# Performance work log

Measured on AMD Instinct MI355X. Metric: run time of the kernel, lower is better.

Reference implementation:

```python
import jax, jax.numpy as jnp
import numpy as np

ALPHA = 0.95   # synaptic current decay, exp(-dt/tau_syn)
BETA = 0.9     # membrane decay, exp(-dt/tau_mem)
THRESHOLD = 0.0


def setup_inputs() -> dict:
    key = jax.random.key(0)
    B, C, H, W, T = 8, 64, 32, 32, 100
    inputs = jax.random.normal(key, (B, C, H, W, T), dtype=jnp.float32)
    return {"inputs": inputs}


def _lif_forward(inputs):
    B, C, H, W, T = inputs.shape
    x = jnp.moveaxis(inputs, -1, 0)  # (T, B, C, H, W): scan over time
    zeros = jnp.zeros((B, C, H, W), dtype=inputs.dtype)

    def step(carry, x_t):
        syn_cur, mem_cur = carry
        # spike when (mem - 1.0) crosses threshold; hard heaviside forward
        out = (mem_cur - 1.0 > THRESHOLD).astype(inputs.dtype)
        syn_next = ALPHA * syn_cur + x_t
        # reset uses detached spike, and accumulates the OLD syn_current
        mem_next = (BETA * mem_cur + syn_cur) * (1.0 - jax.lax.stop_gradient(out))
        return (syn_next, mem_next), (syn_next, mem_next, out)

    _, (syn, mem, spike_out) = jax.lax.scan(step, (zeros, zeros), x)
    # stack back to (B, C, H, W, T)
    syn = jnp.moveaxis(syn, 0, -1)
    mem = jnp.moveaxis(mem, 0, -1)
    spike_out = jnp.moveaxis(spike_out, 0, -1)
    return syn, mem, spike_out


def reference(inputs):
    return _lif_forward(inputs)
```

## Files before the change

kernel.cpp:

```cpp
#include <hip/hip_runtime.h>


typedef float f32x4 __attribute__((ext_vector_type(4)));

constexpr int    T_TOT = 100;
constexpr int    NV4   = 25;
constexpr int    ROW4  = 26;
constexpr int    PPW   = 64;
constexpr double ALPHA = 0.95;
constexpr double BETA  = 0.9;

__device__ __forceinline__ double mul_add_rn64(double a, double b, double c) {
    double p = a * b;
    asm("" : "+v"(p));
    return p + c;
}

#define WAVE_FENCE()  do { __builtin_amdgcn_wave_barrier(); \
                           asm volatile("" ::: "memory"); } while (0)

#define STORE_DENSE(OPTR)                                                     \
    do {                                                                      \
        float* ob = (OPTR) + (size_t)pix0 * T_TOT;                            \
        _Pragma("unroll")                                                     \
        for (int k = 0; k < NV4; ++k) {                                       \
            const int g  = 64 * k + lane;                                     \
            const int ps = g / 25;                                            \
            const int es = g - 25 * ps;                                       \
            const f32x4 v = slab[ps * ROW4 + es];                             \
            *reinterpret_cast<f32x4*>(ob + 4 * (size_t)g) = v;                \
        }                                                                     \
    } while (0)

__global__ __launch_bounds__(64)
void lif_fwd(const float* __restrict__ in,
             float* __restrict__ syn_o,
             float* __restrict__ mem_o,
             float* __restrict__ spk_o)
{
    __shared__ f32x4 slab[PPW * ROW4];

    const int lane = threadIdx.x;
    const int pix0 = blockIdx.x * PPW;
    const float* ib = in + (size_t)pix0 * T_TOT;

    #pragma unroll
    for (int k = 0; k < NV4; ++k) {
        const int g  = 64 * k + lane;
        const f32x4 v = *reinterpret_cast<const f32x4*>(ib + 4 * (size_t)g);
        const int ps = g / 25;
        const int es = g - 25 * ps;
        slab[ps * ROW4 + es] = v;
    }
    WAVE_FENCE();

    double syn = 0.0, mem = 0.0;
    f32x4 mv[NV4];
    unsigned smask[4] = {0u, 0u, 0u, 0u};

    #pragma unroll
    for (int e = 0; e < NV4; ++e) {
        const f32x4 xv = slab[lane * ROW4 + e];
        f32x4 sv;
        {
            #pragma clang fp contract(off)
            #pragma unroll
            for (int j = 0; j < 4; ++j) {
                const int    t     = 4 * e + j;
                const double x     = (double)xv[j];
                const bool   o     = (mem - 1.0 > 0.0);
                const double om    = o ? 0.0 : 1.0;
                const double mem_n = mul_add_rn64(BETA, mem, syn) * om;
                const double syn_n = mul_add_rn64(ALPHA, syn, x);
                sv[j]    = (float)syn_n;
                mv[e][j] = (float)mem_n;
                smask[t >> 5] |= (o ? 1u : 0u) << (t & 31);
                syn = syn_n; mem = mem_n;
            }
        }
        slab[lane * ROW4 + e] = sv;
    }
    WAVE_FENCE();

    STORE_DENSE(syn_o);
    WAVE_FENCE();

    #pragma unroll
    for (int e = 0; e < NV4; ++e) slab[lane * ROW4 + e] = mv[e];
    WAVE_FENCE();
    STORE_DENSE(mem_o);
    WAVE_FENCE();

    #pragma unroll
    for (int e = 0; e < NV4; ++e) {
        f32x4 v;
        #pragma unroll
        for (int j = 0; j < 4; ++j) {
            const int t = 4 * e + j;
            v[j] = ((smask[t >> 5] >> (t & 31)) & 1u) ? 1.0f : 0.0f;
        }
        slab[lane * ROW4 + e] = v;
    }
    WAVE_FENCE();
    STORE_DENSE(spk_o);
}

extern "C" void kernel_launch(void* const* d_in, const int* in_sizes, int n_in,
                              void* d_out, int out_size, void* d_ws, size_t ws_size,
                              hipStream_t stream) {
    const float* in = (const float*)d_in[0];
    float* out = (float*)d_out;

    const int n    = in_sizes[0];
    const int npix = n / T_TOT;

    float* syn_o = out;
    float* mem_o = out + (size_t)n;
    float* spk_o = out + 2 * (size_t)n;

    dim3 grid(npix / PPW);
    dim3 block(64);
    lif_fwd<<<grid, block, 0, stream>>>(in, syn_o, mem_o, spk_o);
}
```

Before: 166.9 us.

## Use persistent grid-stride blocks with register prefetch of next task input

Launches a fixed grid of 2048 single-wave blocks that loop over pixel tasks in grid-stride fashion. Each block loads the next task's input into registers while it runs the recurrence and stores for the current task. The aim is to hide global load latency and reduce block launch overhead. In exchange, register pressure rises from the prefetch buffer and fewer waves are resident, which may reduce latency hiding.

```diff
diff --git a/kernel.cpp b/kernel.cpp
--- a/kernel.cpp
+++ b/kernel.cpp
@@ -36,73 +36,96 @@
 void lif_fwd(const float* __restrict__ in,
              float* __restrict__ syn_o,
              float* __restrict__ mem_o,
-             float* __restrict__ spk_o)
+             float* __restrict__ spk_o,
+             int ntask)
 {
     __shared__ f32x4 slab[PPW * ROW4];
 
-    const int lane = threadIdx.x;
-    const int pix0 = blockIdx.x * PPW;
-    const float* ib = in + (size_t)pix0 * T_TOT;
+    const int lane   = threadIdx.x;
+    const int stride = gridDim.x;
 
-    #pragma unroll
-    for (int k = 0; k < NV4; ++k) {
-        const int g  = 64 * k + lane;
-        const f32x4 v = *reinterpret_cast<const f32x4*>(ib + 4 * (size_t)g);
-        const int ps = g / 25;
-        const int es = g - 25 * ps;
-        slab[ps * ROW4 + es] = v;
+    int task = blockIdx.x;
+    if (task >= ntask) return;
+
+    f32x4 xb[NV4];
+    {
+        const float* ib = in + (size_t)task * PPW * T_TOT;
+        #pragma unroll
+        for (int k = 0; k < NV4; ++k)
+            xb[k] = *reinterpret_cast<const f32x4*>(ib + 4 * (size_t)(64 * k + lane));
     }
-    WAVE_FENCE();
 
-    double syn = 0.0, mem = 0.0;
-    f32x4 mv[NV4];
-    unsigned smask[4] = {0u, 0u, 0u, 0u};
+    for (; task < ntask; task += stride) {
+        const int pix0 = task * PPW;
 
-    #pragma unroll
-    for (int e = 0; e < NV4; ++e) {
-        const f32x4 xv = slab[lane * ROW4 + e];
-        f32x4 sv;
-        {
-            #pragma clang fp contract(off)
+        #pragma unroll
+        for (int k = 0; k < NV4; ++k) {
+            const int g  = 64 * k + lane;
+            const int ps = g / 25;
+            const int es = g - 25 * ps;
+            slab[ps * ROW4 + es] = xb[k];
+        }
+        WAVE_FENCE();
+
+        const int nt = task + stride;
+        if (nt < ntask) {
+            const float* ib = in + (size_t)nt * PPW * T_TOT;
+            #pragma unroll
+            for (int k = 0; k < NV4; ++k)
+                xb[k] = *reinterpret_cast<const f32x4*>(ib + 4 * (size_t)(64 * k + lane));
+        }
+
+        double syn = 0.0, mem = 0.0;
+        f32x4 mv[NV4];
+        unsigned smask[4] = {0u, 0u, 0u, 0u};
+
+        #pragma unroll
+        for (int e = 0; e < NV4; ++e) {
+            const f32x4 xv = slab[lane * ROW4 + e];
+            f32x4 sv;
+            {
+                #pragma clang fp contract(off)
+                #pragma unroll
+                for (int j = 0; j < 4; ++j) {
+                    const int    t     = 4 * e + j;
+                    const double x     = (double)xv[j];
+                    const bool   o     = (mem - 1.0 > 0.0);
+                    const double om    = o ? 0.0 : 1.0;
+                    const double mem_n = mul_add_rn64(BETA, mem, syn) * om;
+                    const double syn_n = mul_add_rn64(ALPHA, syn, x);
+                    sv[j]    = (float)syn_n;
+                    mv[e][j] = (float)mem_n;
+                    smask[t >> 5] |= (o ? 1u : 0u) << (t & 31);
+                    syn = syn_n; mem = mem_n;
+                }
+            }
+            slab[lane * ROW4 + e] = sv;
+        }
+        WAVE_FENCE();
+
+        STORE_DENSE(syn_o);
+        WAVE_FENCE();
+
+        #pragma unroll
+        for (int e = 0; e < NV4; ++e) slab[lane * ROW4 + e] = mv[e];
+        WAVE_FENCE();
+        STORE_DENSE(mem_o);
+        WAVE_FENCE();
+
+        #pragma unroll
+        for (int e = 0; e < NV4; ++e) {
+            f32x4 v;
             #pragma unroll
             for (int j = 0; j < 4; ++j) {
-                const int    t     = 4 * e + j;
-                const double x     = (double)xv[j];
-                const bool   o     = (mem - 1.0 > 0.0);
-                const double om    = o ? 0.0 : 1.0;
-                const double mem_n = mul_add_rn64(BETA, mem, syn) * om;
-                const double syn_n = mul_add_rn64(ALPHA, syn, x);
-                sv[j]    = (float)syn_n;
-                mv[e][j] = (float)mem_n;
-                smask[t >> 5] |= (o ? 1u : 0u) << (t & 31);
-                syn = syn_n; mem = mem_n;
+                const int t = 4 * e + j;
+                v[j] = ((smask[t >> 5] >> (t & 31)) & 1u) ? 1.0f : 0.0f;
             }
+            slab[lane * ROW4 + e] = v;
         }
-        slab[lane * ROW4 + e] = sv;
+        WAVE_FENCE();
+        STORE_DENSE(spk_o);
+        WAVE_FENCE();
     }
-    WAVE_FENCE();
-
-    STORE_DENSE(syn_o);
-    WAVE_FENCE();
-
-    #pragma unroll
-    for (int e = 0; e < NV4; ++e) slab[lane * ROW4 + e] = mv[e];
-    WAVE_FENCE();
-    STORE_DENSE(mem_o);
-    WAVE_FENCE();
-
-    #pragma unroll
-    for (int e = 0; e < NV4; ++e) {
-        f32x4 v;
-        #pragma unroll
-        for (int j = 0; j < 4; ++j) {
-            const int t = 4 * e + j;
-            v[j] = ((smask[t >> 5] >> (t & 31)) & 1u) ? 1.0f : 0.0f;
-        }
-        slab[lane * ROW4 + e] = v;
-    }
-    WAVE_FENCE();
-    STORE_DENSE(spk_o);
 }
 
 extern "C" void kernel_launch(void* const* d_in, const int* in_sizes, int n_in,
@@ -111,14 +134,15 @@
     const float* in = (const float*)d_in[0];
     float* out = (float*)d_out;
 
-    const int n    = in_sizes[0];
-    const int npix = n / T_TOT;
+    const int n     = in_sizes[0];
+    const int npix  = n / T_TOT;
+    const int ntask = npix / PPW;
 
     float* syn_o = out;
     float* mem_o = out + (size_t)n;
     float* spk_o = out + 2 * (size_t)n;
 
-    dim3 grid(npix / PPW);
+    dim3 grid(2048);
     dim3 block(64);
-    lif_fwd<<<grid, block, 0, stream>>>(in, syn_o, mem_o, spk_o);
+    lif_fwd<<<grid, block, 0, stream>>>(in, syn_o, mem_o, spk_o, ntask);
 }
```

Measured after the change: 175.5 us. 5.1% more time.
